# Optimization experiments

Measured on AMD Instinct MI355X. Metric: run time of the kernel, lower is better.

The kernel has to match this reference:

```python
import jax, jax.numpy as jnp
import numpy as np
import math

LATENT = 64
COMP = 20
EM_ITERS = 5
GAMMA1 = 1.0  # 1/sqrt(gamma), gamma=1
LOG_NORM_C = -0.5 * math.log(2.0 * math.pi)


def setup_inputs() -> dict:
    key = jax.random.key(0)
    k1, k2, k3 = jax.random.split(key, 3)
    z = jax.random.normal(k1, (64, 8192, LATENT), dtype=jnp.float32)
    # small causal adjacency so (I - A) and the inverses are well conditioned
    A = jax.random.normal(k2, (LATENT, LATENT), dtype=jnp.float32) * 0.05
    init_idx = jax.random.randint(k3, (64, COMP), 0, 8192)
    return {"z": z, "A": A, "init_idx": init_idx}


def _em_step(X, pi, mean, trace, IA):
    # X: [B,N,L], pi/trace: [B,K], mean: [B,K,L], IA = I - A: [L,L]
    B, N, L = X.shape
    # gaussian_log_prob(X, mean) with logvar=0, summed over L, expanded as
    # -0.5*||x-m||^2 + L*c, computed without materializing a [B,N,K,L] tensor
    sq_x = jnp.sum(X * X, axis=-1)                      # [B,N]
    sq_m = jnp.sum(mean * mean, axis=-1)                # [B,K]
    cross = jnp.einsum('bnl,bkl->bnk', X, mean)         # [B,N,K]
    term_x = -0.5 * (sq_x[:, :, None] - 2.0 * cross + sq_m[:, None, :]) + L * LOG_NORM_C
    # gaussian_log_prob(causal(mean), 0, logvar=log(trace) broadcast over L)
    cm = jnp.einsum('bkl,lm->bkm', mean, IA)            # causal(mean)
    lt = jnp.log(trace)                                  # [B,K]
    term_c = -0.5 * (L * lt + jnp.sum(cm * cm, axis=-1) / trace) + L * LOG_NORM_C
    ll = term_x + jnp.log(pi)[:, None, :] + term_c[:, None, :]   # [B,N,K]
    post = jax.nn.softmax(ll, axis=-1)
    Nk = jnp.sum(post, axis=1)                           # [B,K]
    Nk = jnp.where(Nk == 0.0, jnp.asarray(1e-22, Nk.dtype), Nk)
    new_trace = GAMMA1 * jnp.ones_like(Nk)
    # std_causal = causal(I*trace) = trace*(I-A); trace is gamma1 for every
    # (b,k), so the [B,K,L,L] inverse collapses to one shared [L,L] inverse.
    I = jnp.eye(L, dtype=X.dtype)
    M = jnp.linalg.inv(I + (GAMMA1 ** 2) * (IA @ IA.T))
    new_pi = Nk / jnp.sum(Nk, axis=-1, keepdims=True)    # fix_pi=False
    new_mean = jnp.einsum('bnk,bnl->bkl', post, X) / Nk[:, :, None]
    new_mean = jnp.einsum('bkl,lm->bkm', new_mean, M)
    return new_pi, new_mean, new_trace


def reference(z, A, init_idx):
    # EM-based Gaussian-mixture prior (get_unsupervised_prior) of GMVAE
    B, N, L = z.shape
    I = jnp.eye(L, dtype=z.dtype)
    IA = I - A  # linear CausalEncoder: causal(x) = x @ (I - A)
    pi = jnp.full((B, COMP), 1.0 / COMP, dtype=z.dtype)
    trace = jnp.ones((B, COMP), dtype=z.dtype)
    # initial inverse: inv(I + (1/trace) * sig_cas @ sig_cas.T), trace == 1
    M0 = jnp.linalg.inv(I + IA @ IA.T)
    mean = jnp.take_along_axis(z, init_idx[:, :, None], axis=1)  # [B,K,L]
    mean = jnp.einsum('bkl,lm->bkm', mean, M0)
    for _ in range(EM_ITERS):
        pi, mean, trace = _em_step(z, pi, mean, trace, IA)
    return pi, mean, trace
```

## Files before the change

### kernel.cpp

```cpp
#include <hip/hip_runtime.h>
#include <math.h>

#define BB 64
#define NN 8192
#define LL 64
#define KK 20
#define TILE 128
#define NT 8
#define CHUNKS 8
#define ZSB 72
#define ZTS 140
#define PTTS 136
#define NSS 68

typedef float f32x4 __attribute__((ext_vector_type(4)));
typedef short s16x8 __attribute__((ext_vector_type(8)));
typedef short s16x4 __attribute__((ext_vector_type(4)));
typedef unsigned short u16x4 __attribute__((ext_vector_type(4)));
typedef unsigned short u16x2 __attribute__((ext_vector_type(2)));

#define MFMA_BF16 __builtin_amdgcn_mfma_f32_16x16x32_bf16

__device__ __forceinline__ unsigned short f2bf(float f) {
    unsigned int u = __float_as_uint(f);
    u += 0x7fffu + ((u >> 16) & 1u);
    return (unsigned short)(u >> 16);
}
__device__ __forceinline__ float bf2f(unsigned short h) {
    return __uint_as_float(((unsigned int)h) << 16);
}


__global__ __launch_bounds__(256) void k_setup(const float* __restrict__ A,
                                               float* __restrict__ IA,
                                               float* __restrict__ M) {
    __shared__ __align__(16) float sS[64][NSS];
    __shared__ __align__(16) float sXa[64][NSS];
    __shared__ __align__(16) float sXb[64][NSS];
    __shared__ __align__(16) float sT[64][NSS];
    __shared__ float rowsum[64];
    __shared__ float alpha_s;
    int t = threadIdx.x;
    int r0 = (t >> 4) << 2;
    int c0 = (t & 15) << 2;

    for (int i = t; i < 4096; i += 256) {
        int r = i >> 6, c = i & 63;
        float v = (r == c ? 1.0f : 0.0f) - A[i];
        IA[i] = v;
        sT[c][r] = v;
    }
    __syncthreads();
    {
        float s[4][4];
        #pragma unroll
        for (int a = 0; a < 4; ++a)
            #pragma unroll
            for (int b = 0; b < 4; ++b) s[a][b] = 0.f;
        #pragma unroll 4
        for (int l = 0; l < 64; ++l) {
            float4 u = *(const float4*)&sT[l][r0];
            float4 v = *(const float4*)&sT[l][c0];
            float uu[4] = {u.x, u.y, u.z, u.w};
            float vv[4] = {v.x, v.y, v.z, v.w};
            #pragma unroll
            for (int a = 0; a < 4; ++a)
                #pragma unroll
                for (int b = 0; b < 4; ++b) s[a][b] += uu[a] * vv[b];
        }
        #pragma unroll
        for (int a = 0; a < 4; ++a) {
            int r = r0 + a;
            float4 w;
            w.x = s[a][0] + (r == c0 + 0 ? 1.f : 0.f);
            w.y = s[a][1] + (r == c0 + 1 ? 1.f : 0.f);
            w.z = s[a][2] + (r == c0 + 2 ? 1.f : 0.f);
            w.w = s[a][3] + (r == c0 + 3 ? 1.f : 0.f);
            *(float4*)&sS[r][c0] = w;
        }
    }
    __syncthreads();
    if (t < 64) {
        float sm = 0.f;
        #pragma unroll 4
        for (int c = 0; c < 64; c += 4) {
            float4 v = *(const float4*)&sS[t][c];
            sm += fabsf(v.x) + fabsf(v.y) + fabsf(v.z) + fabsf(v.w);
        }
        rowsum[t] = sm;
    }
    __syncthreads();
    if (t == 0) {
        float mx = rowsum[0];
        for (int i = 1; i < 64; ++i) mx = fmaxf(mx, rowsum[i]);
        alpha_s = 2.0f / (1.0f + mx);
    }
    __syncthreads();
    float alpha = alpha_s;
    for (int i = t; i < 4096; i += 256) {
        int r = i >> 6, c = i & 63;
        sXa[r][c] = (r == c) ? alpha : 0.f;
    }
    __syncthreads();

    float* X  = &sXa[0][0];
    float* Xn = &sXb[0][0];
    for (int it = 0; it < 8; ++it) {
        {
            float s[4][4];
            #pragma unroll
            for (int a = 0; a < 4; ++a)
                #pragma unroll
                for (int b = 0; b < 4; ++b) s[a][b] = 0.f;
            #pragma unroll 4
            for (int k = 0; k < 64; ++k) {
                float4 u = *(const float4*)&sS[k][r0];
                float4 v = *(const float4*)&X[k * NSS + c0];
                float uu[4] = {u.x, u.y, u.z, u.w};
                float vv[4] = {v.x, v.y, v.z, v.w};
                #pragma unroll
                for (int a = 0; a < 4; ++a)
                    #pragma unroll
                    for (int b = 0; b < 4; ++b) s[a][b] += uu[a] * vv[b];
            }
            #pragma unroll
            for (int a = 0; a < 4; ++a)
                *(float4*)&sT[r0 + a][c0] = (float4){s[a][0], s[a][1], s[a][2], s[a][3]};
        }
        __syncthreads();
        {
            float s[4][4];
            #pragma unroll
            for (int a = 0; a < 4; ++a)
                #pragma unroll
                for (int b = 0; b < 4; ++b) s[a][b] = 0.f;
            #pragma unroll 4
            for (int k = 0; k < 64; ++k) {
                float4 u = *(const float4*)&X[k * NSS + r0];
                float4 v = *(const float4*)&sT[k][c0];
                float uu[4] = {u.x, u.y, u.z, u.w};
                float vv[4] = {v.x, v.y, v.z, v.w};
                #pragma unroll
                for (int a = 0; a < 4; ++a)
                    #pragma unroll
                    for (int b = 0; b < 4; ++b) s[a][b] += uu[a] * vv[b];
            }
            #pragma unroll
            for (int a = 0; a < 4; ++a) {
                float4 xo = *(const float4*)&X[(r0 + a) * NSS + c0];
                float4 w;
                w.x = 2.f * xo.x - s[a][0];
                w.y = 2.f * xo.y - s[a][1];
                w.z = 2.f * xo.z - s[a][2];
                w.w = 2.f * xo.w - s[a][3];
                *(float4*)&Xn[(r0 + a) * NSS + c0] = w;
            }
        }
        __syncthreads();
        float* tmp = X; X = Xn; Xn = tmp;
    }
    for (int i = t; i < 4096; i += 256)
        M[i] = X[(i >> 6) * NSS + (i & 63)];
}

__global__ __launch_bounds__(64) void k_init(const float* __restrict__ z,
                                             const int* __restrict__ idxs,
                                             const float* __restrict__ M,
                                             const float* __restrict__ IA,
                                             float* __restrict__ out_mean,
                                             float* __restrict__ bias,
                                             float* __restrict__ nk,
                                             float* __restrict__ macc,
                                             int* __restrict__ cnt) {
    int k = blockIdx.x, b = blockIdx.y;
    int l = threadIdx.x;
    int bk = b * KK + k;
    __shared__ float srow[64];
    __shared__ float smean[64];
    int idx = idxs[bk];
    srow[l] = z[((size_t)b * NN + idx) * LL + l];
    __syncthreads();
    float nm = 0.f;
    #pragma unroll 8
    for (int m = 0; m < 64; ++m) nm += srow[m] * M[m * 64 + l];
    out_mean[(size_t)bk * LL + l] = nm;
    smean[l] = nm;
    __syncthreads();
    float cm = 0.f;
    #pragma unroll 8
    for (int m = 0; m < 64; ++m) cm += smean[m] * IA[m * 64 + l];
    float sqm = nm * nm;
    float sqc = cm * cm;
    for (int off = 32; off > 0; off >>= 1) {
        sqm += __shfl_down(sqm, off);
        sqc += __shfl_down(sqc, off);
    }
    if (l == 0) {
        bias[bk] = logf(1.0f / KK) - 0.5f * (sqm + sqc);
        nk[bk] = 0.f;
        if (k == 0) cnt[b] = 0;
    }
    macc[(size_t)bk * LL + l] = 0.f;
}

__global__ __launch_bounds__(256, 2) void k_empass(const float* __restrict__ z,
                                                   float* __restrict__ mean,
                                                   float* __restrict__ bias,
                                                   float* __restrict__ nk,
                                                   float* __restrict__ macc,
                                                   int* __restrict__ cnt,
                                                   const float* __restrict__ M,
                                                   const float* __restrict__ IA,
                                                   float* __restrict__ out_pi,
                                                   float* __restrict__ out_trace) {
    __shared__ __align__(16) unsigned short zhl[2][TILE][ZSB];
    __shared__ __align__(16) unsigned short mhl[2][32][ZSB];
    __shared__ __align__(16) unsigned short zT[64][ZTS];
    __shared__ __align__(16) unsigned short ptT[32][PTTS];
    __shared__ __align__(16) float bias_s[32];
    __shared__ float nkred[4][KK];
    __shared__ int isLast;
    int t = threadIdx.x;
    int lane = t & 63;
    int q = t >> 6;
    int ln = lane & 15;
    int lg4 = lane >> 4;
    int b = blockIdx.y;
    size_t zbase = ((size_t)b * NN + (size_t)blockIdx.x * (TILE * NT)) * LL;
    int rbase = 32 * q + 8 * lg4;

    for (int i = t; i < KK * LL; i += 256) {
        float f = mean[(size_t)b * KK * LL + i];
        int k = i >> 6, c = i & 63;
        unsigned short h = f2bf(f);
        mhl[0][k][c] = h;
        mhl[1][k][c] = f2bf(f - bf2f(h));
    }
    for (int i = 20 * ZSB + t; i < 32 * ZSB; i += 256) {
        (&mhl[0][0][0])[i] = 0;
        (&mhl[1][0][0])[i] = 0;
    }
    if (t < 32) bias_s[t] = (t < KK) ? bias[b * KK + t] : -1e30f;
    __syncthreads();
    float4 b0 = *(const float4*)&bias_s[lg4 * 4];
    float4 b1 = *(const float4*)&bias_s[16 + lg4 * 4];
    s16x8 mf[8];
    #pragma unroll
    for (int ks = 0; ks < 2; ++ks) {
        int kc = ks * 32 + lg4 * 8;
        mf[ks * 4 + 0] = *(const s16x8*)&mhl[0][ln][kc];
        mf[ks * 4 + 1] = *(const s16x8*)&mhl[1][ln][kc];
        mf[ks * 4 + 2] = *(const s16x8*)&mhl[0][16 + ln][kc];
        mf[ks * 4 + 3] = *(const s16x8*)&mhl[1][16 + ln][kc];
    }

    const float4* zg = (const float4*)(z + zbase);
    float4 pf[8];

#define LOADT(tt)                                                              \
    {                                                                          \
        _Pragma("unroll")                                                      \
        for (int u = 0; u < 4; ++u) {                                          \
            int r0_ = rbase + 2 * u;                                           \
            pf[2 * u]     = zg[(size_t)(tt) * 2048 + r0_ * 16 + ln];           \
            pf[2 * u + 1] = zg[(size_t)(tt) * 2048 + (r0_ + 1) * 16 + ln];     \
        }                                                                      \
    }
#define WRITE_ZHL                                                              \
    {                                                                          \
        _Pragma("unroll")                                                      \
        for (int u = 0; u < 4; ++u) {                                          \
            int r0_ = rbase + 2 * u;                                           \
            float4 v0 = pf[2 * u], v1 = pf[2 * u + 1];                         \
            unsigned short h0 = f2bf(v0.x), h1 = f2bf(v0.y),                   \
                           h2 = f2bf(v0.z), h3 = f2bf(v0.w);                   \
            unsigned short g0 = f2bf(v1.x), g1 = f2bf(v1.y),                   \
                           g2 = f2bf(v1.z), g3 = f2bf(v1.w);                   \
            *(u16x4*)&zhl[0][r0_][4 * ln]     = (u16x4){h0, h1, h2, h3};       \
            *(u16x4*)&zhl[0][r0_ + 1][4 * ln] = (u16x4){g0, g1, g2, g3};       \
            *(u16x4*)&zhl[1][r0_][4 * ln] =                                    \
                (u16x4){f2bf(v0.x - bf2f(h0)), f2bf(v0.y - bf2f(h1)),          \
                        f2bf(v0.z - bf2f(h2)), f2bf(v0.w - bf2f(h3))};         \
            *(u16x4*)&zhl[1][r0_ + 1][4 * ln] =                                \
                (u16x4){f2bf(v1.x - bf2f(g0)), f2bf(v1.y - bf2f(g1)),          \
                        f2bf(v1.z - bf2f(g2)), f2bf(v1.w - bf2f(g3))};         \
        }                                                                      \
    }
#define WRITE_ZT                                                               \
    {                                                                          \
        _Pragma("unroll")                                                      \
        for (int u = 0; u < 4; ++u) {                                          \
            int r0_ = rbase + 2 * u;                                           \
            float4 v0 = pf[2 * u], v1 = pf[2 * u + 1];                         \
            *(u16x2*)&zT[4 * ln + 0][r0_] = (u16x2){f2bf(v0.x), f2bf(v1.x)};   \
            *(u16x2*)&zT[4 * ln + 1][r0_] = (u16x2){f2bf(v0.y), f2bf(v1.y)};   \
            *(u16x2*)&zT[4 * ln + 2][r0_] = (u16x2){f2bf(v0.z), f2bf(v1.z)};   \
            *(u16x2*)&zT[4 * ln + 3][r0_] = (u16x2){f2bf(v0.w), f2bf(v1.w)};   \
        }                                                                      \
    }

    LOADT(0);
    WRITE_ZHL;
    WRITE_ZT;
    __syncthreads();

    f32x4 bacc0 = {0.f, 0.f, 0.f, 0.f};
    f32x4 bacc1 = {0.f, 0.f, 0.f, 0.f};
    float nkp0[4] = {0.f, 0.f, 0.f, 0.f};
    float nkp1[4] = {0.f, 0.f, 0.f, 0.f};

    for (int tt = 0; tt < NT; ++tt) {
        if (tt + 1 < NT) LOADT(tt + 1);

        f32x4 acc0[2], acc1[2];
        #pragma unroll
        for (int rt = 0; rt < 2; ++rt) {
            acc0[rt] = (f32x4){b0.x, b0.y, b0.z, b0.w};
            acc1[rt] = (f32x4){b1.x, b1.y, b1.z, b1.w};
        }
        #pragma unroll
        for (int ks = 0; ks < 2; ++ks) {
            int kc = ks * 32 + lg4 * 8;
            #pragma unroll
            for (int rt = 0; rt < 2; ++rt) {
                int zrow = q * 32 + rt * 16 + ln;
                s16x8 zh = *(const s16x8*)&zhl[0][zrow][kc];
                s16x8 zl = *(const s16x8*)&zhl[1][zrow][kc];
                acc0[rt] = MFMA_BF16(mf[ks * 4 + 0], zh, acc0[rt], 0, 0, 0);
                acc0[rt] = MFMA_BF16(mf[ks * 4 + 1], zh, acc0[rt], 0, 0, 0);
                acc0[rt] = MFMA_BF16(mf[ks * 4 + 0], zl, acc0[rt], 0, 0, 0);
                acc1[rt] = MFMA_BF16(mf[ks * 4 + 2], zh, acc1[rt], 0, 0, 0);
                acc1[rt] = MFMA_BF16(mf[ks * 4 + 3], zh, acc1[rt], 0, 0, 0);
                acc1[rt] = MFMA_BF16(mf[ks * 4 + 2], zl, acc1[rt], 0, 0, 0);
            }
        }
        #pragma unroll
        for (int rt = 0; rt < 2; ++rt) {
            int zrow = q * 32 + rt * 16 + ln;
            float m = fmaxf(fmaxf(fmaxf(acc0[rt][0], acc0[rt][1]), fmaxf(acc0[rt][2], acc0[rt][3])),
                            fmaxf(fmaxf(acc1[rt][0], acc1[rt][1]), fmaxf(acc1[rt][2], acc1[rt][3])));
            m = fmaxf(m, __shfl_xor(m, 16));
            m = fmaxf(m, __shfl_xor(m, 32));
            float e0[4], e1[4];
            float sm = 0.f;
            #pragma unroll
            for (int j = 0; j < 4; ++j) {
                e0[j] = __expf(acc0[rt][j] - m); sm += e0[j];
                e1[j] = __expf(acc1[rt][j] - m); sm += e1[j];
            }
            sm += __shfl_xor(sm, 16);
            sm += __shfl_xor(sm, 32);
            float inv = 1.0f / sm;
            #pragma unroll
            for (int j = 0; j < 4; ++j) {
                float p0 = e0[j] * inv;
                float p1 = e1[j] * inv;
                nkp0[j] += p0;
                nkp1[j] += p1;
                ptT[lg4 * 4 + j][zrow] = f2bf(p0);
                ptT[16 + lg4 * 4 + j][zrow] = f2bf(p1);
            }
        }
        __syncthreads();

        #pragma unroll
        for (int ch = 0; ch < 4; ++ch) {
            int rr = ch * 32 + lg4 * 8;
            s16x4 zb0 = *(const s16x4*)&zT[q * 16 + ln][rr];
            s16x4 zb1 = *(const s16x4*)&zT[q * 16 + ln][rr + 4];
            s16x8 bfr = (s16x8){zb0[0], zb0[1], zb0[2], zb0[3], zb1[0], zb1[1], zb1[2], zb1[3]};
            s16x8 af0 = *(const s16x8*)&ptT[ln][rr];
            s16x8 af1 = *(const s16x8*)&ptT[16 + ln][rr];
            bacc0 = MFMA_BF16(af0, bfr, bacc0, 0, 0, 0);
            bacc1 = MFMA_BF16(af1, bfr, bacc1, 0, 0, 0);
        }
        if (tt + 1 < NT) WRITE_ZHL;
        __syncthreads();
        if (tt + 1 < NT) WRITE_ZT;
    }

    #pragma unroll
    for (int j = 0; j < 4; ++j) {
        nkp0[j] += __shfl_xor(nkp0[j], 1);
        nkp0[j] += __shfl_xor(nkp0[j], 2);
        nkp0[j] += __shfl_xor(nkp0[j], 4);
        nkp0[j] += __shfl_xor(nkp0[j], 8);
        nkp1[j] += __shfl_xor(nkp1[j], 1);
        nkp1[j] += __shfl_xor(nkp1[j], 2);
        nkp1[j] += __shfl_xor(nkp1[j], 4);
        nkp1[j] += __shfl_xor(nkp1[j], 8);
    }
    if (ln == 0) {
        #pragma unroll
        for (int j = 0; j < 4; ++j) nkred[q][lg4 * 4 + j] = nkp0[j];
        if (lg4 == 0) {
            #pragma unroll
            for (int j = 0; j < 4; ++j) nkred[q][16 + j] = nkp1[j];
        }
    }

    int col = q * 16 + ln;
    #pragma unroll
    for (int reg = 0; reg < 4; ++reg) {
        int comp = lg4 * 4 + reg;
        atomicAdd(&macc[((size_t)b * KK + comp) * LL + col], bacc0[reg]);
    }
    if (lg4 == 0) {
        #pragma unroll
        for (int reg = 0; reg < 4; ++reg)
            atomicAdd(&macc[((size_t)b * KK + 16 + reg) * LL + col], bacc1[reg]);
    }
    __syncthreads();
    if (t < KK) {
        float sum = nkred[0][t] + nkred[1][t] + nkred[2][t] + nkred[3][t];
        atomicAdd(&nk[b * KK + t], sum);
    }
    __syncthreads();
    if (t == 0) {
        __threadfence();
        int old = atomicAdd(&cnt[b], 1);
        isLast = (old == CHUNKS - 1) ? 1 : 0;
    }
    __syncthreads();
    if (!isLast) return;

    float* fs = (float*)&zhl[0][0][0];
    float* sraw = fs + q * 160;
    float* smean = sraw + 64;
    int l = lane;
    #pragma unroll
    for (int kc5 = 0; kc5 < 5; ++kc5) {
        int comp = kc5 * 4 + q;
        int bk = b * KK + comp;
        size_t mb = (size_t)bk * LL;
        float nkv = 0.f;
        if (l == 0) nkv = atomicExch(&nk[bk], 0.f);
        nkv = __shfl(nkv, 0);
        float nkc = fmaxf(nkv, 1e-22f);
        float raw = atomicExch(&macc[mb + l], 0.f) / nkc;
        sraw[l] = raw;
        float nm = 0.f;
        #pragma unroll 8
        for (int m = 0; m < 64; ++m) nm += sraw[m] * M[m * 64 + l];
        mean[mb + l] = nm;
        smean[l] = nm;
        float cm = 0.f;
        #pragma unroll 8
        for (int m = 0; m < 64; ++m) cm += smean[m] * IA[m * 64 + l];
        float sqm = nm * nm;
        float sqc = cm * cm;
        #pragma unroll
        for (int off = 32; off > 0; off >>= 1) {
            sqm += __shfl_down(sqm, off);
            sqc += __shfl_down(sqc, off);
        }
        if (l == 0) {
            float pi = nkc * (1.0f / NN);
            bias[bk] = logf(pi) - 0.5f * (sqm + sqc);
            out_pi[bk] = pi;
            out_trace[bk] = 1.0f;
        }
    }
    if (t == 0) cnt[b] = 0;
#undef LOADT
#undef WRITE_ZHL
#undef WRITE_ZT
}

extern "C" void kernel_launch(void* const* d_in, const int* in_sizes, int n_in,
                              void* d_out, int out_size, void* d_ws, size_t ws_size,
                              hipStream_t stream) {
    const float* z = (const float*)d_in[0];
    const float* A = (const float*)d_in[1];
    const int* idxs = (const int*)d_in[2];

    float* out_pi = (float*)d_out;
    float* out_mean = out_pi + BB * KK;
    float* out_trace = out_mean + (size_t)BB * KK * LL;

    float* ws = (float*)d_ws;
    float* IA = ws;
    float* M = ws + 4096;
    float* bias = ws + 8192;
    float* nk = ws + 9472;
    float* macc = ws + 10752;
    int* cnt = (int*)(ws + 92672);

    k_setup<<<1, 256, 0, stream>>>(A, IA, M);
    k_init<<<dim3(KK, BB), 64, 0, stream>>>(z, idxs, M, IA, out_mean, bias, nk, macc, cnt);
    for (int it = 0; it < 5; ++it) {
        k_empass<<<dim3(CHUNKS, BB), 256, 0, stream>>>(z, out_mean, bias, nk, macc,
                                                       cnt, M, IA, out_pi, out_trace);
    }
}
```

Measured before the change: 335.0 us.

## Feed MFMA directly from registers and use 512-thread blocks in EM pass

The E-step now builds the bf16 hi/lo split of z straight into MFMA operand registers instead of staging it in a zhl shared-memory tile. Blocks grow to 512 threads, with 8 waves each handling 16 rows per tile. The M-step accumulation is split across waves by column tile and chunk half. This removes the zhl LDS round trip and raises the wave count per block, with the aim of more memory-latency hiding. In exchange it needs a larger launch bound and more per-wave reductions, and it reduces the software prefetch depth per thread.

```diff
diff --git a/kernel.cpp b/kernel.cpp
--- a/kernel.cpp
+++ b/kernel.cpp
@@ -9,15 +9,12 @@
 #define NT 8
 #define CHUNKS 8
 #define ZSB 72
-#define ZTS 140
+#define ZTS 136
 #define PTTS 136
 #define NSS 68
 
 typedef float f32x4 __attribute__((ext_vector_type(4)));
 typedef short s16x8 __attribute__((ext_vector_type(8)));
-typedef short s16x4 __attribute__((ext_vector_type(4)));
-typedef unsigned short u16x4 __attribute__((ext_vector_type(4)));
-typedef unsigned short u16x2 __attribute__((ext_vector_type(2)));
 
 #define MFMA_BF16 __builtin_amdgcn_mfma_f32_16x16x32_bf16
 
@@ -203,7 +200,7 @@
     macc[(size_t)bk * LL + l] = 0.f;
 }
 
-__global__ __launch_bounds__(256, 2) void k_empass(const float* __restrict__ z,
+__global__ __launch_bounds__(512, 4) void k_empass(const float* __restrict__ z,
                                                    float* __restrict__ mean,
                                                    float* __restrict__ bias,
                                                    float* __restrict__ nk,
@@ -213,12 +210,11 @@
                                                    const float* __restrict__ IA,
                                                    float* __restrict__ out_pi,
                                                    float* __restrict__ out_trace) {
-    __shared__ __align__(16) unsigned short zhl[2][TILE][ZSB];
     __shared__ __align__(16) unsigned short mhl[2][32][ZSB];
     __shared__ __align__(16) unsigned short zT[64][ZTS];
     __shared__ __align__(16) unsigned short ptT[32][PTTS];
     __shared__ __align__(16) float bias_s[32];
-    __shared__ float nkred[4][KK];
+    __shared__ float nkred[8][KK];
     __shared__ int isLast;
     int t = threadIdx.x;
     int lane = t & 63;
@@ -227,20 +223,28 @@
     int lg4 = lane >> 4;
     int b = blockIdx.y;
     size_t zbase = ((size_t)b * NN + (size_t)blockIdx.x * (TILE * NT)) * LL;
-    int rbase = 32 * q + 8 * lg4;
-
-    for (int i = t; i < KK * LL; i += 256) {
+    int zr = q * 16 + ln;
+    int fbase = zr * 16 + 2 * lg4;
+
+    for (int i = t; i < KK * LL; i += 512) {
         float f = mean[(size_t)b * KK * LL + i];
         int k = i >> 6, c = i & 63;
         unsigned short h = f2bf(f);
         mhl[0][k][c] = h;
         mhl[1][k][c] = f2bf(f - bf2f(h));
     }
-    for (int i = 20 * ZSB + t; i < 32 * ZSB; i += 256) {
+    for (int i = 20 * ZSB + t; i < 32 * ZSB; i += 512) {
         (&mhl[0][0][0])[i] = 0;
         (&mhl[1][0][0])[i] = 0;
     }
     if (t < 32) bias_s[t] = (t < KK) ? bias[b * KK + t] : -1e30f;
+
+    const float4* zg = (const float4*)(z + zbase);
+    float4 pf[4];
+    pf[0] = zg[fbase];
+    pf[1] = zg[fbase + 1];
+    pf[2] = zg[fbase + 8];
+    pf[3] = zg[fbase + 9];
     __syncthreads();
     float4 b0 = *(const float4*)&bias_s[lg4 * 4];
     float4 b1 = *(const float4*)&bias_s[16 + lg4 * 4];
@@ -254,99 +258,76 @@
         mf[ks * 4 + 3] = *(const s16x8*)&mhl[1][16 + ln][kc];
     }
 
-    const float4* zg = (const float4*)(z + zbase);
-    float4 pf[8];
-
-#define LOADT(tt)                                                              \
-    {                                                                          \
-        _Pragma("unroll")                                                      \
-        for (int u = 0; u < 4; ++u) {                                          \
-            int r0_ = rbase + 2 * u;                                           \
-            pf[2 * u]     = zg[(size_t)(tt) * 2048 + r0_ * 16 + ln];           \
-            pf[2 * u + 1] = zg[(size_t)(tt) * 2048 + (r0_ + 1) * 16 + ln];     \
-        }                                                                      \
-    }
-#define WRITE_ZHL                                                              \
-    {                                                                          \
-        _Pragma("unroll")                                                      \
-        for (int u = 0; u < 4; ++u) {                                          \
-            int r0_ = rbase + 2 * u;                                           \
-            float4 v0 = pf[2 * u], v1 = pf[2 * u + 1];                         \
-            unsigned short h0 = f2bf(v0.x), h1 = f2bf(v0.y),                   \
-                           h2 = f2bf(v0.z), h3 = f2bf(v0.w);                   \
-            unsigned short g0 = f2bf(v1.x), g1 = f2bf(v1.y),                   \
-                           g2 = f2bf(v1.z), g3 = f2bf(v1.w);                   \
-            *(u16x4*)&zhl[0][r0_][4 * ln]     = (u16x4){h0, h1, h2, h3};       \
-            *(u16x4*)&zhl[0][r0_ + 1][4 * ln] = (u16x4){g0, g1, g2, g3};       \
-            *(u16x4*)&zhl[1][r0_][4 * ln] =                                    \
-                (u16x4){f2bf(v0.x - bf2f(h0)), f2bf(v0.y - bf2f(h1)),          \
-                        f2bf(v0.z - bf2f(h2)), f2bf(v0.w - bf2f(h3))};         \
-            *(u16x4*)&zhl[1][r0_ + 1][4 * ln] =                                \
-                (u16x4){f2bf(v1.x - bf2f(g0)), f2bf(v1.y - bf2f(g1)),          \
-                        f2bf(v1.z - bf2f(g2)), f2bf(v1.w - bf2f(g3))};         \
-        }                                                                      \
-    }
-#define WRITE_ZT                                                               \
-    {                                                                          \
-        _Pragma("unroll")                                                      \
-        for (int u = 0; u < 4; ++u) {                                          \
-            int r0_ = rbase + 2 * u;                                           \
-            float4 v0 = pf[2 * u], v1 = pf[2 * u + 1];                         \
-            *(u16x2*)&zT[4 * ln + 0][r0_] = (u16x2){f2bf(v0.x), f2bf(v1.x)};   \
-            *(u16x2*)&zT[4 * ln + 1][r0_] = (u16x2){f2bf(v0.y), f2bf(v1.y)};   \
-            *(u16x2*)&zT[4 * ln + 2][r0_] = (u16x2){f2bf(v0.z), f2bf(v1.z)};   \
-            *(u16x2*)&zT[4 * ln + 3][r0_] = (u16x2){f2bf(v0.w), f2bf(v1.w)};   \
-        }                                                                      \
-    }
-
-    LOADT(0);
-    WRITE_ZHL;
-    WRITE_ZT;
-    __syncthreads();
-
+    int ct = q & 3;
+    int chb = 2 * (q >> 2);
     f32x4 bacc0 = {0.f, 0.f, 0.f, 0.f};
     f32x4 bacc1 = {0.f, 0.f, 0.f, 0.f};
     float nkp0[4] = {0.f, 0.f, 0.f, 0.f};
     float nkp1[4] = {0.f, 0.f, 0.f, 0.f};
 
     for (int tt = 0; tt < NT; ++tt) {
-        if (tt + 1 < NT) LOADT(tt + 1);
-
-        f32x4 acc0[2], acc1[2];
-        #pragma unroll
-        for (int rt = 0; rt < 2; ++rt) {
-            acc0[rt] = (f32x4){b0.x, b0.y, b0.z, b0.w};
-            acc1[rt] = (f32x4){b1.x, b1.y, b1.z, b1.w};
-        }
-        #pragma unroll
-        for (int ks = 0; ks < 2; ++ks) {
-            int kc = ks * 32 + lg4 * 8;
-            #pragma unroll
-            for (int rt = 0; rt < 2; ++rt) {
-                int zrow = q * 32 + rt * 16 + ln;
-                s16x8 zh = *(const s16x8*)&zhl[0][zrow][kc];
-                s16x8 zl = *(const s16x8*)&zhl[1][zrow][kc];
-                acc0[rt] = MFMA_BF16(mf[ks * 4 + 0], zh, acc0[rt], 0, 0, 0);
-                acc0[rt] = MFMA_BF16(mf[ks * 4 + 1], zh, acc0[rt], 0, 0, 0);
-                acc0[rt] = MFMA_BF16(mf[ks * 4 + 0], zl, acc0[rt], 0, 0, 0);
-                acc1[rt] = MFMA_BF16(mf[ks * 4 + 2], zh, acc1[rt], 0, 0, 0);
-                acc1[rt] = MFMA_BF16(mf[ks * 4 + 3], zh, acc1[rt], 0, 0, 0);
-                acc1[rt] = MFMA_BF16(mf[ks * 4 + 2], zl, acc1[rt], 0, 0, 0);
-            }
-        }
-        #pragma unroll
-        for (int rt = 0; rt < 2; ++rt) {
-            int zrow = q * 32 + rt * 16 + ln;
-            float m = fmaxf(fmaxf(fmaxf(acc0[rt][0], acc0[rt][1]), fmaxf(acc0[rt][2], acc0[rt][3])),
-                            fmaxf(fmaxf(acc1[rt][0], acc1[rt][1]), fmaxf(acc1[rt][2], acc1[rt][3])));
+        s16x8 zh0, zl0, zh1, zl1;
+        #pragma unroll
+        for (int i = 0; i < 2; ++i) {
+            float4 v = pf[i];
+            float vv[4] = {v.x, v.y, v.z, v.w};
+            #pragma unroll
+            for (int j = 0; j < 4; ++j) {
+                unsigned short h = f2bf(vv[j]);
+                zh0[4 * i + j] = (short)h;
+                zl0[4 * i + j] = (short)f2bf(vv[j] - bf2f(h));
+            }
+        }
+        #pragma unroll
+        for (int i = 0; i < 2; ++i) {
+            float4 v = pf[2 + i];
+            float vv[4] = {v.x, v.y, v.z, v.w};
+            #pragma unroll
+            for (int j = 0; j < 4; ++j) {
+                unsigned short h = f2bf(vv[j]);
+                zh1[4 * i + j] = (short)h;
+                zl1[4 * i + j] = (short)f2bf(vv[j] - bf2f(h));
+            }
+        }
+        if (tt + 1 < NT) {
+            size_t o = (size_t)(tt + 1) * 2048;
+            pf[0] = zg[o + fbase];
+            pf[1] = zg[o + fbase + 1];
+            pf[2] = zg[o + fbase + 8];
+            pf[3] = zg[o + fbase + 9];
+        }
+        #pragma unroll
+        for (int e = 0; e < 8; ++e) {
+            zT[8 * lg4 + e][zr]      = (unsigned short)zh0[e];
+            zT[32 + 8 * lg4 + e][zr] = (unsigned short)zh1[e];
+        }
+
+        f32x4 acc0 = (f32x4){b0.x, b0.y, b0.z, b0.w};
+        f32x4 acc1 = (f32x4){b1.x, b1.y, b1.z, b1.w};
+        acc0 = MFMA_BF16(mf[0], zh0, acc0, 0, 0, 0);
+        acc0 = MFMA_BF16(mf[1], zh0, acc0, 0, 0, 0);
+        acc0 = MFMA_BF16(mf[0], zl0, acc0, 0, 0, 0);
+        acc0 = MFMA_BF16(mf[4], zh1, acc0, 0, 0, 0);
+        acc0 = MFMA_BF16(mf[5], zh1, acc0, 0, 0, 0);
+        acc0 = MFMA_BF16(mf[4], zl1, acc0, 0, 0, 0);
+        acc1 = MFMA_BF16(mf[2], zh0, acc1, 0, 0, 0);
+        acc1 = MFMA_BF16(mf[3], zh0, acc1, 0, 0, 0);
+        acc1 = MFMA_BF16(mf[2], zl0, acc1, 0, 0, 0);
+        acc1 = MFMA_BF16(mf[6], zh1, acc1, 0, 0, 0);
+        acc1 = MFMA_BF16(mf[7], zh1, acc1, 0, 0, 0);
+        acc1 = MFMA_BF16(mf[6], zl1, acc1, 0, 0, 0);
+
+        {
+            float m = fmaxf(fmaxf(fmaxf(acc0[0], acc0[1]), fmaxf(acc0[2], acc0[3])),
+                            fmaxf(fmaxf(acc1[0], acc1[1]), fmaxf(acc1[2], acc1[3])));
             m = fmaxf(m, __shfl_xor(m, 16));
             m = fmaxf(m, __shfl_xor(m, 32));
             float e0[4], e1[4];
             float sm = 0.f;
             #pragma unroll
             for (int j = 0; j < 4; ++j) {
-                e0[j] = __expf(acc0[rt][j] - m); sm += e0[j];
-                e1[j] = __expf(acc1[rt][j] - m); sm += e1[j];
+                e0[j] = __expf(acc0[j] - m); sm += e0[j];
+                e1[j] = __expf(acc1[j] - m); sm += e1[j];
             }
             sm += __shfl_xor(sm, 16);
             sm += __shfl_xor(sm, 32);
@@ -357,26 +338,22 @@
                 float p1 = e1[j] * inv;
                 nkp0[j] += p0;
                 nkp1[j] += p1;
-                ptT[lg4 * 4 + j][zrow] = f2bf(p0);
-                ptT[16 + lg4 * 4 + j][zrow] = f2bf(p1);
+                ptT[lg4 * 4 + j][zr] = f2bf(p0);
+                ptT[16 + lg4 * 4 + j][zr] = f2bf(p1);
             }
         }
         __syncthreads();
 
         #pragma unroll
-        for (int ch = 0; ch < 4; ++ch) {
-            int rr = ch * 32 + lg4 * 8;
-            s16x4 zb0 = *(const s16x4*)&zT[q * 16 + ln][rr];
-            s16x4 zb1 = *(const s16x4*)&zT[q * 16 + ln][rr + 4];
-            s16x8 bfr = (s16x8){zb0[0], zb0[1], zb0[2], zb0[3], zb1[0], zb1[1], zb1[2], zb1[3]};
+        for (int chi = 0; chi < 2; ++chi) {
+            int rr = (chb + chi) * 32 + lg4 * 8;
+            s16x8 zb  = *(const s16x8*)&zT[ct * 16 + ln][rr];
             s16x8 af0 = *(const s16x8*)&ptT[ln][rr];
             s16x8 af1 = *(const s16x8*)&ptT[16 + ln][rr];
-            bacc0 = MFMA_BF16(af0, bfr, bacc0, 0, 0, 0);
-            bacc1 = MFMA_BF16(af1, bfr, bacc1, 0, 0, 0);
-        }
-        if (tt + 1 < NT) WRITE_ZHL;
+            bacc0 = MFMA_BF16(af0, zb, bacc0, 0, 0, 0);
+            bacc1 = MFMA_BF16(af1, zb, bacc1, 0, 0, 0);
+        }
         __syncthreads();
-        if (tt + 1 < NT) WRITE_ZT;
     }
 
     #pragma unroll
@@ -399,7 +376,7 @@
         }
     }
 
-    int col = q * 16 + ln;
+    int col = ct * 16 + ln;
     #pragma unroll
     for (int reg = 0; reg < 4; ++reg) {
         int comp = lg4 * 4 + reg;
@@ -412,7 +389,9 @@
     }
     __syncthreads();
     if (t < KK) {
-        float sum = nkred[0][t] + nkred[1][t] + nkred[2][t] + nkred[3][t];
+        float sum = 0.f;
+        #pragma unroll
+        for (int w = 0; w < 8; ++w) sum += nkred[w][t];
         atomicAdd(&nk[b * KK + t], sum);
     }
     __syncthreads();
@@ -424,47 +403,46 @@
     __syncthreads();
     if (!isLast) return;
 
-    float* fs = (float*)&zhl[0][0][0];
-    float* sraw = fs + q * 160;
-    float* smean = sraw + 64;
-    int l = lane;
-    #pragma unroll
-    for (int kc5 = 0; kc5 < 5; ++kc5) {
-        int comp = kc5 * 4 + q;
-        int bk = b * KK + comp;
-        size_t mb = (size_t)bk * LL;
-        float nkv = 0.f;
-        if (l == 0) nkv = atomicExch(&nk[bk], 0.f);
-        nkv = __shfl(nkv, 0);
-        float nkc = fmaxf(nkv, 1e-22f);
-        float raw = atomicExch(&macc[mb + l], 0.f) / nkc;
-        sraw[l] = raw;
-        float nm = 0.f;
-        #pragma unroll 8
-        for (int m = 0; m < 64; ++m) nm += sraw[m] * M[m * 64 + l];
-        mean[mb + l] = nm;
-        smean[l] = nm;
-        float cm = 0.f;
-        #pragma unroll 8
-        for (int m = 0; m < 64; ++m) cm += smean[m] * IA[m * 64 + l];
-        float sqm = nm * nm;
-        float sqc = cm * cm;
-        #pragma unroll
-        for (int off = 32; off > 0; off >>= 1) {
-            sqm += __shfl_down(sqm, off);
-            sqc += __shfl_down(sqc, off);
-        }
-        if (l == 0) {
-            float pi = nkc * (1.0f / NN);
-            bias[bk] = logf(pi) - 0.5f * (sqm + sqc);
-            out_pi[bk] = pi;
-            out_trace[bk] = 1.0f;
+    if (q < 4) {
+        float* fs = (float*)&zT[0][0];
+        float* sraw = fs + q * 160;
+        float* smean = sraw + 64;
+        int l = lane;
+        #pragma unroll
+        for (int kc5 = 0; kc5 < 5; ++kc5) {
+            int comp = kc5 * 4 + q;
+            int bk = b * KK + comp;
+            size_t mb = (size_t)bk * LL;
+            float nkv = 0.f;
+            if (l == 0) nkv = atomicExch(&nk[bk], 0.f);
+            nkv = __shfl(nkv, 0);
+            float nkc = fmaxf(nkv, 1e-22f);
+            float raw = atomicExch(&macc[mb + l], 0.f) / nkc;
+            sraw[l] = raw;
+            float nm = 0.f;
+            #pragma unroll 8
+            for (int m = 0; m < 64; ++m) nm += sraw[m] * M[m * 64 + l];
+            mean[mb + l] = nm;
+            smean[l] = nm;
+            float cm = 0.f;
+            #pragma unroll 8
+            for (int m = 0; m < 64; ++m) cm += smean[m] * IA[m * 64 + l];
+            float sqm = nm * nm;
+            float sqc = cm * cm;
+            #pragma unroll
+            for (int off = 32; off > 0; off >>= 1) {
+                sqm += __shfl_down(sqm, off);
+                sqc += __shfl_down(sqc, off);
+            }
+            if (l == 0) {
+                float pi = nkc * (1.0f / NN);
+                bias[bk] = logf(pi) - 0.5f * (sqm + sqc);
+                out_pi[bk] = pi;
+                out_trace[bk] = 1.0f;
+            }
         }
     }
     if (t == 0) cnt[b] = 0;
-#undef LOADT
-#undef WRITE_ZHL
-#undef WRITE_ZT
 }
 
 extern "C" void kernel_launch(void* const* d_in, const int* in_sizes, int n_in,
@@ -489,7 +467,7 @@
     k_setup<<<1, 256, 0, stream>>>(A, IA, M);
     k_init<<<dim3(KK, BB), 64, 0, stream>>>(z, idxs, M, IA, out_mean, bias, nk, macc, cnt);
     for (int it = 0; it < 5; ++it) {
-        k_empass<<<dim3(CHUNKS, BB), 256, 0, stream>>>(z, out_mean, bias, nk, macc,
+        k_empass<<<dim3(CHUNKS, BB), 512, 0, stream>>>(z, out_mean, bias, nk, macc,
                                                        cnt, M, IA, out_pi, out_trace);
     }
 }
```

New measurement: 306.7 us. 8.5% less time.
